# Optimization experiments

Hardware: AMD Instinct MI355X
Metric: run time of the kernel (lower is better)

## Reference

```python
import jax, jax.numpy as jnp
import numpy as np

B, S, D, F, H, E = 2, 1024, 1024, 4096, 16, 8
EPS = 1e-5


def _layernorm(x, w, b):
    m = jnp.mean(x, -1, keepdims=True)
    v = jnp.var(x, -1, keepdims=True)
    return (x - m) * jax.lax.rsqrt(v + EPS) * w + b


def _rope(x):
    # rotary embedding applied over full embed dim (split-half convention)
    b, s, d = x.shape
    half = d // 2
    inv = 1.0 / (10000.0 ** (jnp.arange(half, dtype=jnp.float32) / half))
    ang = jnp.arange(s, dtype=jnp.float32)[:, None] * inv[None, :]  # [S, half]
    cos, sin = jnp.cos(ang), jnp.sin(ang)
    x1, x2 = x[..., :half], x[..., half:]
    return jnp.concatenate([x1 * cos - x2 * sin, x1 * sin + x2 * cos], -1)


def setup_inputs() -> dict:
    key = jax.random.key(0)
    ks = jax.random.split(key, 9)
    sc = 0.02
    return {
        "x": jax.random.normal(ks[0], (B, S, D), jnp.float32),
        "ln1_w": jnp.ones((D,), jnp.float32),
        "ln1_b": jnp.zeros((D,), jnp.float32),
        "ln2_w": jnp.ones((D,), jnp.float32),
        "ln2_b": jnp.zeros((D,), jnp.float32),
        "w_qkv": jax.random.normal(ks[1], (3 * D, D), jnp.float32) * sc,
        "b_qkv": jnp.zeros((3 * D,), jnp.float32),
        "w_out": jax.random.normal(ks[2], (D, D), jnp.float32) * sc,
        "b_out": jnp.zeros((D,), jnp.float32),
        "w_router": jax.random.normal(ks[3], (D, E), jnp.float32) * sc,
        "wi": jax.random.normal(ks[4], (E, D, F), jnp.float32) * sc,  # per-expert wi (no bias)
        "wo": jax.random.normal(ks[5], (E, F // 2, D), jnp.float32) * sc,  # swiglu halves ffn dim
    }


def reference(x, ln1_w, ln1_b, ln2_w, ln2_b, w_qkv, b_qkv, w_out, b_out, w_router, wi, wo):
    # ---- pre-norm self-attention block ----
    residual = x
    h = _layernorm(x, ln1_w, ln1_b)
    h = _rope(h)
    qkv = h @ w_qkv.T + b_qkv  # [B,S,3D]
    q, k, v = jnp.split(qkv, 3, axis=-1)
    hd = D // H
    to_heads = lambda t: t.reshape(B, S, H, hd).transpose(0, 2, 1, 3)
    q, k, v = to_heads(q), to_heads(k), to_heads(v)
    scale = 1.0 / np.sqrt(hd).astype(np.float32)
    att = jax.nn.softmax(jnp.einsum('bhqd,bhkd->bhqk', q, k) * scale, axis=-1)
    o = jnp.einsum('bhqk,bhkd->bhqd', att, v).transpose(0, 2, 1, 3).reshape(B, S, D)
    o = o @ w_out.T + b_out
    x = residual + o  # attn dropout is identity at eval

    # ---- pre-norm sparse MoE FFN block ----
    residual = x
    h = _layernorm(x, ln2_w, ln2_b)
    # top-1 router in float32
    logits = h.astype(jnp.float32) @ w_router  # [B,S,E]
    probs = jax.nn.softmax(logits, axis=-1)
    mask = jax.nn.one_hot(jnp.argmax(probs, -1), E, dtype=h.dtype)  # expert_mask
    gate = probs.astype(h.dtype) * mask  # router_probs * expert_mask, [B,S,E]
    # dense all-expert compute, masked combine (same math as gather/scatter loop)
    hid = jnp.einsum('bsd,edf->bsef', h, wi)  # [B,S,E,F]
    a, g = jnp.split(hid, 2, axis=-1)
    act = jax.nn.silu(a) * g  # SwiGLU, [B,S,E,F/2]
    y = jnp.einsum('bsef,efd,bse->bsd', act, wo, gate)
    x = residual + y
    return x, logits
```

## Files before the change

kernel.cpp:

```cpp
#include <hip/hip_runtime.h>
#include <hip/hip_bf16.h>
#include <math.h>

#define BB 2
#define SS 1024
#define DD 1024
#define FF 4096
#define HH 16
#define EE 8
#define MM (BB*SS)
#define MAX_TILES 24
#define MAX_TILES2 40

typedef __attribute__((ext_vector_type(8))) short bf16x8;
typedef __attribute__((ext_vector_type(8))) short s16x8;
typedef __attribute__((ext_vector_type(4))) float f32x4;

#define OFF_WQH  ((size_t)100663296)
#define OFF_WQL  ((size_t)106954752)
#define OFF_WOH  ((size_t)113246208)
#define OFF_WOL  ((size_t)115343360)
#define OFF_H1H  ((size_t)117440512)
#define OFF_H1L  ((size_t)121634816)
#define OFF_QKV  ((size_t)125829120)
#define OFF_OH   ((size_t)150994944)
#define OFF_OL   ((size_t)155189248)
#define OFF_X2   ((size_t)159383552)
#define OFF_H2B  ((size_t)167772160)
#define OFF_ACT  ((size_t)171966464)
#define OFF_GATE ((size_t)180879360)
#define OFF_EID  ((size_t)180887552)
#define OFF_PERM ((size_t)180895744)
#define OFF_CNT  ((size_t)180903936)
#define OFF_FILL ((size_t)180903968)
#define OFF_NT   ((size_t)180904000)
#define OFF_TE   ((size_t)180904192)
#define OFF_TS   ((size_t)180904320)
#define OFF_TR   ((size_t)180904448)
#define OFF_TE2  ((size_t)180904576)
#define OFF_TS2  ((size_t)180904768)
#define OFF_TR2  ((size_t)180904960)
#define OFF_NT2  ((size_t)180905152)
#define OFF_KSH  OFF_WQH
#define OFF_KSL  (OFF_WQH + 4194304)
#define OFF_VTH  OFF_H1H
#define OFF_VTL  OFF_H1L

__device__ __forceinline__ void gload16(const void* g, void* l) {
    __builtin_amdgcn_global_load_lds(
        (const __attribute__((address_space(1))) unsigned int*)g,
        (__attribute__((address_space(3))) unsigned int*)l, 16, 0, 0);
}

__device__ __forceinline__ short bfh(float v) {
    __hip_bfloat16 h = __float2bfloat16(v);
    return *(short*)&h;
}
__device__ __forceinline__ float bf2f(short s) {
    __hip_bfloat16 h = *(__hip_bfloat16*)&s;
    return __bfloat162float(h);
}

__device__ __forceinline__ void split_write(float v, __hip_bfloat16* hp, __hip_bfloat16* lp, size_t idx) {
    __hip_bfloat16 h = __float2bfloat16(v);
    hp[idx] = h;
    lp[idx] = __float2bfloat16(v - __bfloat162float(h));
}

__global__ void k_phase0(const float* __restrict__ x, const float* __restrict__ ln1w,
                         const float* __restrict__ ln1b,
                         __hip_bfloat16* __restrict__ h1H, __hip_bfloat16* __restrict__ h1L,
                         const float* __restrict__ w_qkv, __hip_bfloat16* __restrict__ wqH,
                         __hip_bfloat16* __restrict__ wqL,
                         const float* __restrict__ w_out, __hip_bfloat16* __restrict__ woH,
                         __hip_bfloat16* __restrict__ woL) {
    __shared__ __align__(16) float smem[1032];
    int bid = blockIdx.x, t = threadIdx.x;
    if (bid < 2048) {
        int m = bid, s = m & (SS - 1);
        float* row = smem;
        float* red = smem + 1024;
        const float* xp = x + (size_t)m * DD;
        float sum = 0.f, sumsq = 0.f;
#pragma unroll
        for (int l = 0; l < 4; ++l) {
            int i = t + l * 256;
            float v = xp[i];
            row[i] = v;
            sum += v; sumsq += v * v;
        }
#pragma unroll
        for (int off = 32; off; off >>= 1) {
            sum   += __shfl_xor(sum, off);
            sumsq += __shfl_xor(sumsq, off);
        }
        int wid = t >> 6, lane = t & 63;
        if (lane == 0) { red[wid] = sum; red[4 + wid] = sumsq; }
        __syncthreads();
        sum   = red[0] + red[1] + red[2] + red[3];
        sumsq = red[4] + red[5] + red[6] + red[7];
        float mean = sum * (1.f / DD);
        float var  = sumsq * (1.f / DD) - mean * mean;
        float rstd = rsqrtf(var + 1e-5f);
        size_t base = (size_t)m * DD;
        const float kln = logf(10000.f) / 512.f;
#pragma unroll
        for (int l = 0; l < 2; ++l) {
            int i = t + l * 256;
            float n1 = (row[i]       - mean) * rstd * ln1w[i]       + ln1b[i];
            float n2 = (row[i + 512] - mean) * rstd * ln1w[i + 512] + ln1b[i + 512];
            float inv = expf(-(float)i * kln);
            float ang = (float)s * inv;
            float c = cosf(ang), sn = sinf(ang);
            split_write(n1 * c - n2 * sn,  h1H, h1L, base + i);
            split_write(n1 * sn + n2 * c, h1H, h1L, base + i + 512);
        }
    } else if (bid < 5120) {
        int idx = (bid - 2048) * 256 + t;
        float4 v = ((const float4*)w_qkv)[idx];
        split_write(v.x, wqH, wqL, (size_t)idx * 4 + 0);
        split_write(v.y, wqH, wqL, (size_t)idx * 4 + 1);
        split_write(v.z, wqH, wqL, (size_t)idx * 4 + 2);
        split_write(v.w, wqH, wqL, (size_t)idx * 4 + 3);
    } else {
        int idx = (bid - 5120) * 256 + t;
        float4 v = ((const float4*)w_out)[idx];
        split_write(v.x, woH, woL, (size_t)idx * 4 + 0);
        split_write(v.y, woH, woL, (size_t)idx * 4 + 1);
        split_write(v.z, woH, woL, (size_t)idx * 4 + 2);
        split_write(v.w, woH, woL, (size_t)idx * 4 + 3);
    }
}

__global__ void k_qkv(const __hip_bfloat16* __restrict__ Ah, const __hip_bfloat16* __restrict__ Al,
                      const __hip_bfloat16* __restrict__ Bh, const __hip_bfloat16* __restrict__ Bl,
                      const float* __restrict__ bias, float* __restrict__ Cf) {
    __shared__ __align__(16) short AsH[64 * 32];
    __shared__ __align__(16) short AsL[64 * 32];
    __shared__ __align__(16) short BsH[128 * 32];
    __shared__ __align__(16) short BsL[128 * 32];
    const int N = 3072, K = DD;
    int bid = blockIdx.x;
    int xcd = bid & 7, idx = bid >> 3;
    int nt = xcd + (idx >> 5) * 8;
    int mt = idx & 31;
    int m0 = mt * 64, n0 = nt * 128;
    const int t = threadIdx.x;
    const int w = t >> 6, lane = t & 63;
    const int sid = w * 64 + lane;
    const int g = lane >> 4, r16 = lane & 15;

    f32x4 acc[4][2] = {};

    for (int k0 = 0; k0 < K; k0 += 32) {
        {
            int rrow = sid >> 2, sl = sid & 3;
            int slog = sl ^ ((rrow >> 1) & 3);
            size_t lbase = (size_t)(w * 64) * 8;
            size_t gaoff = (size_t)(m0 + rrow) * K + k0 + slog * 8;
            gload16(Ah + gaoff, &AsH[lbase]);
            gload16(Al + gaoff, &AsL[lbase]);
        }
#pragma unroll
        for (int j = 0; j < 2; ++j) {
            int id = j * 256 + sid;
            int rrow = id >> 2, sl = id & 3;
            int slog = sl ^ ((rrow >> 1) & 3);
            size_t lbase = (size_t)(j * 256 + w * 64) * 8;
            size_t gboff = (size_t)(n0 + rrow) * K + k0 + slog * 8;
            gload16(Bh + gboff, &BsH[lbase]);
            gload16(Bl + gboff, &BsL[lbase]);
        }
        __syncthreads();
        bf16x8 ah[4], al[4], bh[2], bl[2];
#pragma unroll
        for (int i = 0; i < 4; ++i) {
            int ra = i * 16 + r16;
            int pa = g ^ ((ra >> 1) & 3);
            ah[i] = *(const bf16x8*)&AsH[ra * 32 + pa * 8];
            al[i] = *(const bf16x8*)&AsL[ra * 32 + pa * 8];
        }
#pragma unroll
        for (int n = 0; n < 2; ++n) {
            int rb = w * 32 + n * 16 + r16;
            int pb = g ^ ((rb >> 1) & 3);
            bh[n] = *(const bf16x8*)&BsH[rb * 32 + pb * 8];
            bl[n] = *(const bf16x8*)&BsL[rb * 32 + pb * 8];
        }
#pragma unroll
        for (int i = 0; i < 4; ++i)
#pragma unroll
            for (int n = 0; n < 2; ++n) {
                acc[i][n] = __builtin_amdgcn_mfma_f32_16x16x32_bf16(ah[i], bh[n], acc[i][n], 0, 0, 0);
                acc[i][n] = __builtin_amdgcn_mfma_f32_16x16x32_bf16(ah[i], bl[n], acc[i][n], 0, 0, 0);
                acc[i][n] = __builtin_amdgcn_mfma_f32_16x16x32_bf16(al[i], bh[n], acc[i][n], 0, 0, 0);
            }
        __syncthreads();
    }

#pragma unroll
    for (int i = 0; i < 4; ++i) {
#pragma unroll
        for (int n = 0; n < 2; ++n) {
            int col = n0 + w * 32 + n * 16 + r16;
#pragma unroll
            for (int q = 0; q < 4; ++q) {
                int r = m0 + i * 16 + g * 4 + q;
                Cf[(size_t)r * N + col] = acc[i][n][q] + bias[col];
            }
        }
    }
}

__global__ void k_oproj64(const __hip_bfloat16* __restrict__ Ah, const __hip_bfloat16* __restrict__ Al,
                          const __hip_bfloat16* __restrict__ Bh, const __hip_bfloat16* __restrict__ Bl,
                          const float* __restrict__ bias, const float* __restrict__ addsrc,
                          float* __restrict__ Cf, int* __restrict__ zero17) {
    __shared__ __align__(16) short AsH[64 * 32];
    __shared__ __align__(16) short AsL[64 * 32];
    __shared__ __align__(16) short BsH[128 * 32];
    __shared__ __align__(16) short BsL[128 * 32];
    const int N = DD, K = DD;
    int bid = blockIdx.x;
    int m0 = (bid >> 3) * 64, n0 = (bid & 7) * 128;
    const int t = threadIdx.x;
    if (bid == 0 && t < 17) zero17[t] = 0;
    const int w = t >> 6, lane = t & 63;
    const int sid = w * 64 + lane;
    const int g = lane >> 4, r16 = lane & 15;

    f32x4 acc[4][2] = {};

    for (int k0 = 0; k0 < K; k0 += 32) {
        {
            int rrow = sid >> 2, sl = sid & 3;
            int slog = sl ^ ((rrow >> 1) & 3);
            size_t lbase = (size_t)(w * 64) * 8;
            size_t gaoff = (size_t)(m0 + rrow) * K + k0 + slog * 8;
            gload16(Ah + gaoff, &AsH[lbase]);
            gload16(Al + gaoff, &AsL[lbase]);
        }
#pragma unroll
        for (int j = 0; j < 2; ++j) {
            int id = j * 256 + sid;
            int rrow = id >> 2, sl = id & 3;
            int slog = sl ^ ((rrow >> 1) & 3);
            size_t lbase = (size_t)(j * 256 + w * 64) * 8;
            size_t gboff = (size_t)(n0 + rrow) * K + k0 + slog * 8;
            gload16(Bh + gboff, &BsH[lbase]);
            gload16(Bl + gboff, &BsL[lbase]);
        }
        __syncthreads();
        bf16x8 ah[4], al[4], bh[2], bl[2];
#pragma unroll
        for (int i = 0; i < 4; ++i) {
            int ra = i * 16 + r16;
            int pa = g ^ ((ra >> 1) & 3);
            ah[i] = *(const bf16x8*)&AsH[ra * 32 + pa * 8];
            al[i] = *(const bf16x8*)&AsL[ra * 32 + pa * 8];
        }
#pragma unroll
        for (int n = 0; n < 2; ++n) {
            int rb = w * 32 + n * 16 + r16;
            int pb = g ^ ((rb >> 1) & 3);
            bh[n] = *(const bf16x8*)&BsH[rb * 32 + pb * 8];
            bl[n] = *(const bf16x8*)&BsL[rb * 32 + pb * 8];
        }
#pragma unroll
        for (int i = 0; i < 4; ++i)
#pragma unroll
            for (int n = 0; n < 2; ++n) {
                acc[i][n] = __builtin_amdgcn_mfma_f32_16x16x32_bf16(ah[i], bh[n], acc[i][n], 0, 0, 0);
                acc[i][n] = __builtin_amdgcn_mfma_f32_16x16x32_bf16(ah[i], bl[n], acc[i][n], 0, 0, 0);
                acc[i][n] = __builtin_amdgcn_mfma_f32_16x16x32_bf16(al[i], bh[n], acc[i][n], 0, 0, 0);
            }
        __syncthreads();
    }

#pragma unroll
    for (int i = 0; i < 4; ++i) {
#pragma unroll
        for (int n = 0; n < 2; ++n) {
            int col = n0 + w * 32 + n * 16 + r16;
#pragma unroll
            for (int q = 0; q < 4; ++q) {
                int r = m0 + i * 16 + g * 4 + q;
                Cf[(size_t)r * N + col] =
                    acc[i][n][q] + bias[col] + addsrc[(size_t)r * N + col];
            }
        }
    }
}

#define LDB 36
__global__ void k_moe_up(const __hip_bfloat16* __restrict__ A,
                         const float* __restrict__ wi,
                         __hip_bfloat16* __restrict__ act,
                         const int* __restrict__ perm,
                         const int* __restrict__ te, const int* __restrict__ ts,
                         const int* __restrict__ tr, const int* __restrict__ ntl) {
    __shared__ __align__(16) short As[128 * 32];
    __shared__ __align__(16) short Bs[128 * LDB];
    __shared__ int permS[128];
    int tile = blockIdx.y;
    if (tile >= *ntl) return;
    int e = te[tile], rs = ts[tile], rows = tr[tile];
    const int t = threadIdx.x;
    if (t < 128) permS[t] = (t < rows) ? perm[rs + t] : 0;
    __syncthreads();
    int c0 = blockIdx.x * 64;
    const int w = t >> 6, lane = t & 63;
    const int wr = w >> 1, wc = w & 1;
    const int sid = w * 64 + lane;
    const int g = lane >> 4, r16 = lane & 15;

    const float* Bp = wi + (size_t)e * DD * FF;

    const int cc = t & 127, kp0 = t >> 7;
    const int Lc = cc & 63, T = cc >> 6;
    const int qidx = (Lc >> 5) * 4 + ((Lc >> 4) & 1) * 2 + T;
    const int rbb = qidx * 16 + (Lc & 15);
    const size_t coloff = (size_t)(c0 + T * 2048 + Lc);

    f32x4 acc[4][4] = {};

    float vcur[16];
#pragma unroll
    for (int pass = 0; pass < 8; ++pass) {
        int kp = pass * 2 + kp0;
        const float* wp = Bp + (size_t)(kp * 2) * FF + coloff;
        vcur[pass * 2]     = wp[0];
        vcur[pass * 2 + 1] = wp[FF];
    }

    for (int k0 = 0; k0 < DD; k0 += 32) {
#pragma unroll
        for (int j = 0; j < 2; ++j) {
            int id = j * 256 + sid;
            int rrow = id >> 2, sl = id & 3;
            int slog = sl ^ ((rrow >> 1) & 3);
            size_t lbase = (size_t)(j * 256 + w * 64) * 8;
            gload16(A + (size_t)permS[rrow] * DD + k0 + slog * 8, &As[lbase]);
        }
#pragma unroll
        for (int pass = 0; pass < 8; ++pass) {
            int kp = pass * 2 + kp0;
            unsigned u = (unsigned)(unsigned short)bfh(vcur[pass * 2])
                       | ((unsigned)(unsigned short)bfh(vcur[pass * 2 + 1]) << 16);
            *(unsigned*)&Bs[rbb * LDB + kp * 2] = u;
        }
        __syncthreads();
        float vnext[16];
        if (k0 + 32 < DD) {
#pragma unroll
            for (int pass = 0; pass < 8; ++pass) {
                int kp = pass * 2 + kp0;
                const float* wp = Bp + (size_t)(k0 + 32 + kp * 2) * FF + coloff;
                vnext[pass * 2]     = wp[0];
                vnext[pass * 2 + 1] = wp[FF];
            }
        }
        bf16x8 af[4];
#pragma unroll
        for (int i = 0; i < 4; ++i) {
            int ra = wr * 64 + i * 16 + r16;
            int pa = g ^ ((ra >> 1) & 3);
            af[i] = *(const bf16x8*)&As[ra * 32 + pa * 8];
        }
        bf16x8 bfr[4];
#pragma unroll
        for (int n = 0; n < 4; ++n) {
            int rb = wc * 64 + n * 16 + r16;
            bfr[n] = *(const bf16x8*)&Bs[rb * LDB + g * 8];
        }
#pragma unroll
        for (int i = 0; i < 4; ++i)
#pragma unroll
            for (int n = 0; n < 4; ++n)
                acc[i][n] = __builtin_amdgcn_mfma_f32_16x16x32_bf16(af[i], bfr[n], acc[i][n], 0, 0, 0);
        __syncthreads();
        if (k0 + 32 < DD) {
#pragma unroll
            for (int j = 0; j < 16; ++j) vcur[j] = vnext[j];
        }
    }

#pragma unroll
    for (int i = 0; i < 4; ++i) {
#pragma unroll
        for (int p2 = 0; p2 < 2; ++p2) {
            int col = c0 + wc * 32 + p2 * 16 + r16;
#pragma unroll
            for (int q = 0; q < 4; ++q) {
                int r = wr * 64 + i * 16 + g * 4 + q;
                if (r < rows) {
                    float a  = acc[i][2 * p2][q];
                    float gv = acc[i][2 * p2 + 1][q];
                    act[(size_t)(rs + r) * 2048 + col] =
                        __float2bfloat16((a / (1.f + expf(-a))) * gv);
                }
            }
        }
    }
}

__global__ void k_moe_dn(const __hip_bfloat16* __restrict__ A,
                         const float* __restrict__ wo,
                         const float* __restrict__ addsrc, float* __restrict__ Cf,
                         const int* __restrict__ perm,
                         const int* __restrict__ te2, const int* __restrict__ ts2,
                         const int* __restrict__ tr2, const int* __restrict__ ntl2,
                         const float* __restrict__ gate) {
    __shared__ __align__(16) short As[64 * 32];
    __shared__ __align__(16) short Bs[64 * LDB];
    __shared__ int permS[64];
    int tile = blockIdx.y;
    if (tile >= *ntl2) return;
    int e = te2[tile], rs = ts2[tile], rows = tr2[tile];
    const int t = threadIdx.x;
    if (t < 64) permS[t] = (t < rows) ? perm[rs + t] : 0;
    __syncthreads();
    int n0 = blockIdx.x * 64;
    const int w = t >> 6, lane = t & 63;
    const int sid = w * 64 + lane;
    const int g = lane >> 4, r16 = lane & 15;
    const int K = FF / 2;

    const float* Bp = wo + (size_t)e * (size_t)K * DD;
    const int cc = t & 63, kp0 = t >> 6;

    f32x4 acc[4] = {};

    float vcur[8];
#pragma unroll
    for (int pass = 0; pass < 4; ++pass) {
        int kp = pass * 4 + kp0;
        const float* wp = Bp + (size_t)(kp * 2) * DD + n0 + cc;
        vcur[pass * 2]     = wp[0];
        vcur[pass * 2 + 1] = wp[DD];
    }

    for (int k0 = 0; k0 < K; k0 += 32) {
        {
            int rrow = sid >> 2, sl = sid & 3;
            int slog = sl ^ ((rrow >> 1) & 3);
            size_t lbase = (size_t)(w * 64) * 8;
            gload16(A + (size_t)(rs + rrow) * K + k0 + slog * 8, &As[lbase]);
        }
#pragma unroll
        for (int pass = 0; pass < 4; ++pass) {
            int kp = pass * 4 + kp0;
            unsigned u = (unsigned)(unsigned short)bfh(vcur[pass * 2])
                       | ((unsigned)(unsigned short)bfh(vcur[pass * 2 + 1]) << 16);
            *(unsigned*)&Bs[cc * LDB + kp * 2] = u;
        }
        __syncthreads();
        float vnext[8];
        if (k0 + 32 < K) {
#pragma unroll
            for (int pass = 0; pass < 4; ++pass) {
                int kp = pass * 4 + kp0;
                const float* wp = Bp + (size_t)(k0 + 32 + kp * 2) * DD + n0 + cc;
                vnext[pass * 2]     = wp[0];
                vnext[pass * 2 + 1] = wp[DD];
            }
        }
        bf16x8 af[4], bfr;
#pragma unroll
        for (int i = 0; i < 4; ++i) {
            int ra = i * 16 + r16;
            int pa = g ^ ((ra >> 1) & 3);
            af[i] = *(const bf16x8*)&As[ra * 32 + pa * 8];
        }
        {
            int rb = w * 16 + r16;
            bfr = *(const bf16x8*)&Bs[rb * LDB + g * 8];
        }
#pragma unroll
        for (int i = 0; i < 4; ++i)
            acc[i] = __builtin_amdgcn_mfma_f32_16x16x32_bf16(af[i], bfr, acc[i], 0, 0, 0);
        __syncthreads();
        if (k0 + 32 < K) {
#pragma unroll
            for (int j = 0; j < 8; ++j) vcur[j] = vnext[j];
        }
    }

#pragma unroll
    for (int i = 0; i < 4; ++i) {
        int col = n0 + w * 16 + r16;
#pragma unroll
        for (int q = 0; q < 4; ++q) {
            int r = i * 16 + g * 4 + q;
            if (r >= rows) continue;
            int tok = permS[r];
            Cf[(size_t)tok * DD + col] = addsrc[(size_t)tok * DD + col] + gate[tok] * acc[i][q];
        }
    }
}

__global__ void k_prep(const float* __restrict__ qkv, short* __restrict__ KH, short* __restrict__ KL,
                       short* __restrict__ VH, short* __restrict__ VL) {
    __shared__ float tile[64][65];
    int b = blockIdx.z, h = blockIdx.y, s0 = blockIdx.x * 64;
    int t = threadIdx.x;
    int row = t >> 2, c0 = (t & 3) * 16;
    const float* kp = qkv + (size_t)(b * SS + s0 + row) * 3072 + 1024 + h * 64 + c0;
    const float* vp = kp + 1024;
    {
        size_t krow = ((size_t)(b * HH + h) * SS + s0 + row) * 64;
        int key = (s0 + row) & 7;
#pragma unroll
        for (int g2 = 0; g2 < 2; ++g2) {
            s16x8 hv, lv;
#pragma unroll
            for (int j = 0; j < 8; ++j) {
                float v = kp[g2 * 8 + j];
                short hh = bfh(v);
                hv[j] = hh; lv[j] = bfh(v - bf2f(hh));
            }
            int p = ((c0 >> 3) + g2) ^ key;
            *(s16x8*)&KH[krow + p * 8] = hv;
            *(s16x8*)&KL[krow + p * 8] = lv;
        }
    }
#pragma unroll
    for (int j = 0; j < 16; ++j) tile[row][c0 + j] = vp[j];
    __syncthreads();
    {
        int d = t >> 2, sc = (t & 3) * 16;
        size_t vrow = ((size_t)(b * HH + h) * 64 + d) * SS + s0;
        int key = d & 7;
#pragma unroll
        for (int g2 = 0; g2 < 2; ++g2) {
            s16x8 hv, lv;
#pragma unroll
            for (int j = 0; j < 8; ++j) {
                float v = tile[sc + g2 * 8 + j][d];
                short hh = bfh(v);
                hv[j] = hh; lv[j] = bfh(v - bf2f(hh));
            }
            int p = ((sc >> 3) + g2) ^ key;
            *(s16x8*)&VH[vrow + p * 8] = hv;
            *(s16x8*)&VL[vrow + p * 8] = lv;
        }
    }
}

#define LDP 72
__global__ __launch_bounds__(512, 1)
void k_attn_mfma(const float* __restrict__ qkv,
                 const short* __restrict__ KH, const short* __restrict__ KL,
                 const short* __restrict__ VH, const short* __restrict__ VL,
                 __hip_bfloat16* __restrict__ ohi, __hip_bfloat16* __restrict__ olo) {
    __shared__ __align__(16) short Ks[2][64 * 64], Kl2[2][64 * 64], Vs[2][64 * 64], Vl2[2][64 * 64];
    __shared__ __align__(16) short PhS[8][16 * LDP], PlS[8][16 * LDP];
    int id = blockIdx.x;
    int xcd = id & 7, slot = id >> 3;
    int bh = xcd * 4 + (slot >> 3);
    int q0 = (slot & 7) * 128;
    int b = bh >> 4, h = bh & 15;
    int t = threadIdx.x;
    int w = t >> 6, lane = t & 63;
    int g = lane >> 4, r16 = lane & 15;
    int srow = t >> 3, sslot = t & 7;

    const size_t kbase = ((size_t)bh * SS) * 64;
    const size_t vbase = ((size_t)bh * 64) * SS;

    bf16x8 qfh[2], qfl[2];
    {
        const float* qp = qkv + (size_t)(b * SS + q0 + w * 16 + r16) * 3072 + h * 64;
#pragma unroll
        for (int ks = 0; ks < 2; ++ks) {
            float vv[8];
            *(float4*)&vv[0] = *(const float4*)(qp + ks * 32 + g * 8);
            *(float4*)&vv[4] = *(const float4*)(qp + ks * 32 + g * 8 + 4);
#pragma unroll
            for (int j = 0; j < 8; ++j) {
                float sv = vv[j] * 0.125f;
                short hh = bfh(sv);
                qfh[ks][j] = hh;
                qfl[ks][j] = bfh(sv - bf2f(hh));
            }
        }
    }

    float mrun[4], lrun[4];
    f32x4 oacc[4] = {};
#pragma unroll
    for (int q = 0; q < 4; ++q) { mrun[q] = -1e30f; lrun[q] = 0.f; }

    gload16(KH + kbase + (size_t)srow * 64 + sslot * 8, &Ks[0][w * 512]);
    gload16(KL + kbase + (size_t)srow * 64 + sslot * 8, &Kl2[0][w * 512]);
    gload16(VH + vbase + (size_t)srow * SS + sslot * 8, &Vs[0][w * 512]);
    gload16(VL + vbase + (size_t)srow * SS + sslot * 8, &Vl2[0][w * 512]);
    __syncthreads();

    int cur = 0;
    for (int k0 = 0; k0 < SS; k0 += 64) {
        if (k0 + 64 < SS) {
            int kn = k0 + 64;
            gload16(KH + kbase + (size_t)(kn + srow) * 64 + sslot * 8, &Ks[cur ^ 1][w * 512]);
            gload16(KL + kbase + (size_t)(kn + srow) * 64 + sslot * 8, &Kl2[cur ^ 1][w * 512]);
            gload16(VH + vbase + (size_t)srow * SS + kn + sslot * 8,   &Vs[cur ^ 1][w * 512]);
            gload16(VL + vbase + (size_t)srow * SS + kn + sslot * 8,   &Vl2[cur ^ 1][w * 512]);
        }

        f32x4 accs[4] = {};
#pragma unroll
        for (int ks = 0; ks < 2; ++ks) {
            bf16x8 kfh[4], kfl[4];
#pragma unroll
            for (int n = 0; n < 4; ++n) {
                int rb = n * 16 + r16;
                int p = (ks * 4 + g) ^ (r16 & 7);
                kfh[n] = *(const bf16x8*)&Ks[cur][rb * 64 + p * 8];
                kfl[n] = *(const bf16x8*)&Kl2[cur][rb * 64 + p * 8];
            }
            __builtin_amdgcn_s_setprio(1);
#pragma unroll
            for (int n = 0; n < 4; ++n) {
                accs[n] = __builtin_amdgcn_mfma_f32_16x16x32_bf16(qfh[ks], kfh[n], accs[n], 0, 0, 0);
                accs[n] = __builtin_amdgcn_mfma_f32_16x16x32_bf16(qfh[ks], kfl[n], accs[n], 0, 0, 0);
                accs[n] = __builtin_amdgcn_mfma_f32_16x16x32_bf16(qfl[ks], kfh[n], accs[n], 0, 0, 0);
            }
            __builtin_amdgcn_s_setprio(0);
        }

        float mn[4], corr[4], psum[4];
#pragma unroll
        for (int q = 0; q < 4; ++q) {
            float m = fmaxf(fmaxf(accs[0][q], accs[1][q]), fmaxf(accs[2][q], accs[3][q]));
            m = fmaxf(m, __shfl_xor(m, 1));
            m = fmaxf(m, __shfl_xor(m, 2));
            m = fmaxf(m, __shfl_xor(m, 4));
            m = fmaxf(m, __shfl_xor(m, 8));
            mn[q] = fmaxf(mrun[q], m);
            corr[q] = expf(mrun[q] - mn[q]);
            mrun[q] = mn[q];
            psum[q] = 0.f;
        }
#pragma unroll
        for (int n = 0; n < 4; ++n)
#pragma unroll
            for (int q = 0; q < 4; ++q) {
                float p = expf(accs[n][q] - mn[q]);
                psum[q] += p;
                short ph = bfh(p);
                PhS[w][(g * 4 + q) * LDP + n * 16 + r16] = ph;
                PlS[w][(g * 4 + q) * LDP + n * 16 + r16] = bfh(p - bf2f(ph));
            }
#pragma unroll
        for (int q = 0; q < 4; ++q) {
            psum[q] += __shfl_xor(psum[q], 1);
            psum[q] += __shfl_xor(psum[q], 2);
            psum[q] += __shfl_xor(psum[q], 4);
            psum[q] += __shfl_xor(psum[q], 8);
            lrun[q] = lrun[q] * corr[q] + psum[q];
#pragma unroll
            for (int n = 0; n < 4; ++n) oacc[n][q] *= corr[q];
        }

#pragma unroll
        for (int ks = 0; ks < 2; ++ks) {
            bf16x8 vfh[4], vfl[4];
#pragma unroll
            for (int n = 0; n < 4; ++n) {
                int rb = n * 16 + r16;
                int p = (ks * 4 + g) ^ (r16 & 7);
                vfh[n] = *(const bf16x8*)&Vs[cur][rb * 64 + p * 8];
                vfl[n] = *(const bf16x8*)&Vl2[cur][rb * 64 + p * 8];
            }
            bf16x8 pfh = *(const bf16x8*)&PhS[w][r16 * LDP + ks * 32 + g * 8];
            bf16x8 pfl = *(const bf16x8*)&PlS[w][r16 * LDP + ks * 32 + g * 8];
            __builtin_amdgcn_s_setprio(1);
#pragma unroll
            for (int n = 0; n < 4; ++n) {
                oacc[n] = __builtin_amdgcn_mfma_f32_16x16x32_bf16(pfh, vfh[n], oacc[n], 0, 0, 0);
                oacc[n] = __builtin_amdgcn_mfma_f32_16x16x32_bf16(pfh, vfl[n], oacc[n], 0, 0, 0);
                oacc[n] = __builtin_amdgcn_mfma_f32_16x16x32_bf16(pfl, vfh[n], oacc[n], 0, 0, 0);
            }
            __builtin_amdgcn_s_setprio(0);
        }
        __syncthreads();
        cur ^= 1;
    }

    float invl[4];
#pragma unroll
    for (int q = 0; q < 4; ++q) invl[q] = 1.f / lrun[q];
#pragma unroll
    for (int n = 0; n < 4; ++n) {
        int col = h * 64 + n * 16 + r16;
#pragma unroll
        for (int q = 0; q < 4; ++q) {
            int rowg = b * SS + q0 + w * 16 + g * 4 + q;
            split_write(oacc[n][q] * invl[q], ohi, olo, (size_t)rowg * DD + col);
        }
    }
}

__global__ void k_ln2_router(const float* __restrict__ x2, const float* __restrict__ w,
                             const float* __restrict__ b, const float* __restrict__ wr,
                             __hip_bfloat16* __restrict__ h2b, float* __restrict__ logits,
                             float* __restrict__ gate, int* __restrict__ eid,
                             int* __restrict__ counts) {
    int m = blockIdx.x, t = threadIdx.x;
    __shared__ float red[8];
    __shared__ float racc[4][8];
    const float* xp = x2 + (size_t)m * DD;
    float v[4];
    float sum = 0.f, sumsq = 0.f;
#pragma unroll
    for (int l = 0; l < 4; ++l) {
        v[l] = xp[t + l * 256];
        sum += v[l]; sumsq += v[l] * v[l];
    }
#pragma unroll
    for (int off = 32; off; off >>= 1) {
        sum   += __shfl_xor(sum, off);
        sumsq += __shfl_xor(sumsq, off);
    }
    int wid = t >> 6, lane = t & 63;
    if (lane == 0) { red[wid] = sum; red[4 + wid] = sumsq; }
    __syncthreads();
    sum   = red[0] + red[1] + red[2] + red[3];
    sumsq = red[4] + red[5] + red[6] + red[7];
    float mean = sum * (1.f / DD);
    float var  = sumsq * (1.f / DD) - mean * mean;
    float rstd = rsqrtf(var + 1e-5f);
    float acc[EE] = {};
#pragma unroll
    for (int l = 0; l < 4; ++l) {
        int i = t + l * 256;
        float hv = (v[l] - mean) * rstd * w[i] + b[i];
        h2b[(size_t)m * DD + i] = __float2bfloat16(hv);
        const float* wp = wr + (size_t)i * EE;
#pragma unroll
        for (int n = 0; n < EE; ++n) acc[n] += hv * wp[n];
    }
#pragma unroll
    for (int off = 32; off; off >>= 1)
#pragma unroll
        for (int n = 0; n < EE; ++n) acc[n] += __shfl_xor(acc[n], off);
    if (lane == 0)
#pragma unroll
        for (int n = 0; n < EE; ++n) racc[wid][n] = acc[n];
    __syncthreads();
    if (t == 0) {
        float lg[EE];
#pragma unroll
        for (int n = 0; n < EE; ++n) lg[n] = racc[0][n] + racc[1][n] + racc[2][n] + racc[3][n];
        float mx = lg[0]; int best = 0;
#pragma unroll
        for (int n = 1; n < EE; ++n) if (lg[n] > mx) { mx = lg[n]; best = n; }
        float den = 0.f;
#pragma unroll
        for (int n = 0; n < EE; ++n) den += expf(lg[n] - mx);
        gate[m] = 1.f / den;
        eid[m] = best;
        atomicAdd(&counts[best], 1);
#pragma unroll
        for (int n = 0; n < EE; ++n) logits[(size_t)m * EE + n] = lg[n];
    }
}

__global__ void k_offscatter(const int* __restrict__ counts,
                             int* __restrict__ te, int* __restrict__ ts, int* __restrict__ tr,
                             int* __restrict__ ntl,
                             int* __restrict__ te2, int* __restrict__ ts2, int* __restrict__ tr2,
                             int* __restrict__ ntl2,
                             const int* __restrict__ eid,
                             int* __restrict__ fill, int* __restrict__ perm) {
    __shared__ int soffs[EE];
    int t = threadIdx.x;
    if (t == 0) {
        int off = 0, nt = 0, nt2 = 0;
        for (int e = 0; e < EE; ++e) {
            soffs[e] = off;
            int c = counts[e];
            for (int t0 = 0; t0 < c; t0 += 128) {
                te[nt] = e; ts[nt] = off + t0; tr[nt] = (c - t0 < 128) ? (c - t0) : 128; ++nt;
            }
            for (int t0 = 0; t0 < c; t0 += 64) {
                te2[nt2] = e; ts2[nt2] = off + t0; tr2[nt2] = (c - t0 < 64) ? (c - t0) : 64; ++nt2;
            }
            off += c;
        }
        *ntl = nt;
        *ntl2 = nt2;
    }
    __syncthreads();
#pragma unroll
    for (int tok = t; tok < MM; tok += 1024) {
        int e = eid[tok];
        int pos = soffs[e] + atomicAdd(&fill[e], 1);
        perm[pos] = tok;
    }
}

extern "C" void kernel_launch(void* const* d_in, const int* in_sizes, int n_in,
                              void* d_out, int out_size, void* d_ws, size_t ws_size,
                              hipStream_t stream) {
    const float* x     = (const float*)d_in[0];
    const float* ln1w  = (const float*)d_in[1];
    const float* ln1b  = (const float*)d_in[2];
    const float* ln2w  = (const float*)d_in[3];
    const float* ln2b  = (const float*)d_in[4];
    const float* w_qkv = (const float*)d_in[5];
    const float* b_qkv = (const float*)d_in[6];
    const float* w_out = (const float*)d_in[7];
    const float* b_out = (const float*)d_in[8];
    const float* w_rtr = (const float*)d_in[9];
    const float* wi    = (const float*)d_in[10];
    const float* wo    = (const float*)d_in[11];
    float* out = (float*)d_out;

    char* wsb = (char*)d_ws;
    __hip_bfloat16* wqH  = (__hip_bfloat16*)(wsb + OFF_WQH);
    __hip_bfloat16* wqL  = (__hip_bfloat16*)(wsb + OFF_WQL);
    __hip_bfloat16* woH  = (__hip_bfloat16*)(wsb + OFF_WOH);
    __hip_bfloat16* woL  = (__hip_bfloat16*)(wsb + OFF_WOL);
    __hip_bfloat16* h1H  = (__hip_bfloat16*)(wsb + OFF_H1H);
    __hip_bfloat16* h1L  = (__hip_bfloat16*)(wsb + OFF_H1L);
    float*          qkvF = (float*)(wsb + OFF_QKV);
    __hip_bfloat16* oH   = (__hip_bfloat16*)(wsb + OFF_OH);
    __hip_bfloat16* oL   = (__hip_bfloat16*)(wsb + OFF_OL);
    float*          x2F  = (float*)(wsb + OFF_X2);
    __hip_bfloat16* h2B  = (__hip_bfloat16*)(wsb + OFF_H2B);
    __hip_bfloat16* actB = (__hip_bfloat16*)(wsb + OFF_ACT);
    short* KSH = (short*)(wsb + OFF_KSH);
    short* KSL = (short*)(wsb + OFF_KSL);
    short* VTH = (short*)(wsb + OFF_VTH);
    short* VTL = (short*)(wsb + OFF_VTL);
    float* gate = (float*)(wsb + OFF_GATE);
    int* eid    = (int*)(wsb + OFF_EID);
    int* perm   = (int*)(wsb + OFF_PERM);
    int* counts = (int*)(wsb + OFF_CNT);
    int* fill   = (int*)(wsb + OFF_FILL);
    int* ntl    = (int*)(wsb + OFF_NT);
    int* te     = (int*)(wsb + OFF_TE);
    int* tsx    = (int*)(wsb + OFF_TS);
    int* trx    = (int*)(wsb + OFF_TR);
    int* te2    = (int*)(wsb + OFF_TE2);
    int* ts2    = (int*)(wsb + OFF_TS2);
    int* tr2    = (int*)(wsb + OFF_TR2);
    int* ntl2   = (int*)(wsb + OFF_NT2);

    k_phase0<<<6144, 256, 0, stream>>>(x, ln1w, ln1b, h1H, h1L, w_qkv, wqH, wqL,
                                       w_out, woH, woL);
    k_qkv<<<768, 256, 0, stream>>>(h1H, h1L, wqH, wqL, b_qkv, qkvF);
    k_prep<<<dim3(SS / 64, HH, BB), 256, 0, stream>>>(qkvF, KSH, KSL, VTH, VTL);
    k_attn_mfma<<<256, 512, 0, stream>>>(qkvF, KSH, KSL, VTH, VTL, oH, oL);
    k_oproj64<<<256, 256, 0, stream>>>(oH, oL, woH, woL, b_out, x, x2F, counts);
    k_ln2_router<<<MM, 256, 0, stream>>>(x2F, ln2w, ln2b, w_rtr, h2B,
                                         out + (size_t)MM * DD, gate, eid, counts);
    k_offscatter<<<1, 1024, 0, stream>>>(counts, te, tsx, trx, ntl,
                                         te2, ts2, tr2, ntl2, eid, fill, perm);
    k_moe_up<<<dim3(32, MAX_TILES), 256, 0, stream>>>(h2B, wi, actB, perm, te, tsx, trx, ntl);
    k_moe_dn<<<dim3(DD / 64, MAX_TILES2), 256, 0, stream>>>(
        actB, wo, x2F, out, perm, te2, ts2, tr2, ntl2, gate);
}
```

Measured before the change: 331.7 us.

## Use 64-row expert tiles in MoE up-projection and double K-step per barrier

The MoE up-projection switches from 128-row token tiles to the 64-row tile list used by the down-projection. This gives more blocks and less padding waste when experts receive few tokens, but each wi weight tile is now reloaded for more tiles. Both MoE GEMMs now stage 64 K-elements per loop iteration across two LDS panels, halving the number of barriers. The cost is more registers for the prefetched weight values and more shared memory.

Result: faster. 320.9 us (-3.3%).

```diff
diff --git a/kernel.cpp b/kernel.cpp
--- a/kernel.cpp
+++ b/kernel.cpp
@@ -297,21 +297,19 @@
                          const float* __restrict__ wi,
                          __hip_bfloat16* __restrict__ act,
                          const int* __restrict__ perm,
-                         const int* __restrict__ te, const int* __restrict__ ts,
-                         const int* __restrict__ tr, const int* __restrict__ ntl) {
-    __shared__ __align__(16) short As[128 * 32];
-    __shared__ __align__(16) short Bs[128 * LDB];
-    __shared__ int permS[128];
+                         const int* __restrict__ te2, const int* __restrict__ ts2,
+                         const int* __restrict__ tr2, const int* __restrict__ ntl2) {
+    __shared__ __align__(16) short As[2][64 * 32];
+    __shared__ __align__(16) short Bs[2][128 * LDB];
+    __shared__ int permS[64];
     int tile = blockIdx.y;
-    if (tile >= *ntl) return;
-    int e = te[tile], rs = ts[tile], rows = tr[tile];
+    if (tile >= *ntl2) return;
+    int e = te2[tile], rs = ts2[tile], rows = tr2[tile];
     const int t = threadIdx.x;
-    if (t < 128) permS[t] = (t < rows) ? perm[rs + t] : 0;
+    if (t < 64) permS[t] = (t < rows) ? perm[rs + t] : 0;
     __syncthreads();
     int c0 = blockIdx.x * 64;
     const int w = t >> 6, lane = t & 63;
-    const int wr = w >> 1, wc = w & 1;
-    const int sid = w * 64 + lane;
     const int g = lane >> 4, r16 = lane & 15;
 
     const float* Bp = wi + (size_t)e * DD * FF;
@@ -322,80 +320,81 @@
     const int rbb = qidx * 16 + (Lc & 15);
     const size_t coloff = (size_t)(c0 + T * 2048 + Lc);
 
-    f32x4 acc[4][4] = {};
-
-    float vcur[16];
-#pragma unroll
-    for (int pass = 0; pass < 8; ++pass) {
-        int kp = pass * 2 + kp0;
-        const float* wp = Bp + (size_t)(kp * 2) * FF + coloff;
+    f32x4 acc[4][2] = {};
+
+    float vcur[32];
+#pragma unroll
+    for (int pass = 0; pass < 16; ++pass) {
+        int kpg = pass * 2 + kp0;
+        const float* wp = Bp + (size_t)(kpg * 2) * FF + coloff;
         vcur[pass * 2]     = wp[0];
         vcur[pass * 2 + 1] = wp[FF];
     }
 
-    for (int k0 = 0; k0 < DD; k0 += 32) {
+    for (int k0 = 0; k0 < DD; k0 += 64) {
 #pragma unroll
         for (int j = 0; j < 2; ++j) {
-            int id = j * 256 + sid;
-            int rrow = id >> 2, sl = id & 3;
+            int rrow = t >> 2, sl = t & 3;
             int slog = sl ^ ((rrow >> 1) & 3);
-            size_t lbase = (size_t)(j * 256 + w * 64) * 8;
-            gload16(A + (size_t)permS[rrow] * DD + k0 + slog * 8, &As[lbase]);
-        }
-#pragma unroll
-        for (int pass = 0; pass < 8; ++pass) {
-            int kp = pass * 2 + kp0;
+            size_t lbase = (size_t)(w * 64) * 8;
+            gload16(A + (size_t)permS[rrow] * DD + k0 + j * 32 + slog * 8, &As[j][lbase]);
+        }
+#pragma unroll
+        for (int pass = 0; pass < 16; ++pass) {
+            int kpg = pass * 2 + kp0;
+            int panel = kpg >> 4, kpl = kpg & 15;
             unsigned u = (unsigned)(unsigned short)bfh(vcur[pass * 2])
                        | ((unsigned)(unsigned short)bfh(vcur[pass * 2 + 1]) << 16);
-            *(unsigned*)&Bs[rbb * LDB + kp * 2] = u;
-        }
-        __syncthreads();
-        float vnext[16];
-        if (k0 + 32 < DD) {
-#pragma unroll
-            for (int pass = 0; pass < 8; ++pass) {
-                int kp = pass * 2 + kp0;
-                const float* wp = Bp + (size_t)(k0 + 32 + kp * 2) * FF + coloff;
+            *(unsigned*)&Bs[panel][rbb * LDB + kpl * 2] = u;
+        }
+        __syncthreads();
+        float vnext[32];
+        if (k0 + 64 < DD) {
+#pragma unroll
+            for (int pass = 0; pass < 16; ++pass) {
+                int kpg = pass * 2 + kp0;
+                const float* wp = Bp + (size_t)(k0 + 64 + kpg * 2) * FF + coloff;
                 vnext[pass * 2]     = wp[0];
                 vnext[pass * 2 + 1] = wp[FF];
             }
         }
-        bf16x8 af[4];
+#pragma unroll
+        for (int ks = 0; ks < 2; ++ks) {
+            bf16x8 af[4], bf[2];
+#pragma unroll
+            for (int i = 0; i < 4; ++i) {
+                int ra = i * 16 + r16;
+                int pa = g ^ ((ra >> 1) & 3);
+                af[i] = *(const bf16x8*)&As[ks][ra * 32 + pa * 8];
+            }
+#pragma unroll
+            for (int n = 0; n < 2; ++n) {
+                int rb = w * 32 + n * 16 + r16;
+                bf[n] = *(const bf16x8*)&Bs[ks][rb * LDB + g * 8];
+            }
+#pragma unroll
+            for (int i = 0; i < 4; ++i)
+#pragma unroll
+                for (int n = 0; n < 2; ++n)
+                    acc[i][n] = __builtin_amdgcn_mfma_f32_16x16x32_bf16(af[i], bf[n], acc[i][n], 0, 0, 0);
+        }
+        __syncthreads();
+        if (k0 + 64 < DD) {
+#pragma unroll
+            for (int j = 0; j < 32; ++j) vcur[j] = vnext[j];
+        }
+    }
+
+    {
+        int col = c0 + (w >> 1) * 32 + (w & 1) * 16 + r16;
 #pragma unroll
         for (int i = 0; i < 4; ++i) {
-            int ra = wr * 64 + i * 16 + r16;
-            int pa = g ^ ((ra >> 1) & 3);
-            af[i] = *(const bf16x8*)&As[ra * 32 + pa * 8];
-        }
-        bf16x8 bfr[4];
-#pragma unroll
-        for (int n = 0; n < 4; ++n) {
-            int rb = wc * 64 + n * 16 + r16;
-            bfr[n] = *(const bf16x8*)&Bs[rb * LDB + g * 8];
-        }
-#pragma unroll
-        for (int i = 0; i < 4; ++i)
-#pragma unroll
-            for (int n = 0; n < 4; ++n)
-                acc[i][n] = __builtin_amdgcn_mfma_f32_16x16x32_bf16(af[i], bfr[n], acc[i][n], 0, 0, 0);
-        __syncthreads();
-        if (k0 + 32 < DD) {
-#pragma unroll
-            for (int j = 0; j < 16; ++j) vcur[j] = vnext[j];
-        }
-    }
-
-#pragma unroll
-    for (int i = 0; i < 4; ++i) {
-#pragma unroll
-        for (int p2 = 0; p2 < 2; ++p2) {
-            int col = c0 + wc * 32 + p2 * 16 + r16;
 #pragma unroll
             for (int q = 0; q < 4; ++q) {
-                int r = wr * 64 + i * 16 + g * 4 + q;
+                int r = i * 16 + g * 4 + q;
                 if (r < rows) {
-                    float a  = acc[i][2 * p2][q];
-                    float gv = acc[i][2 * p2 + 1][q];
+                    float a  = acc[i][0][q];
+                    float gv = acc[i][1][q];
                     act[(size_t)(rs + r) * 2048 + col] =
                         __float2bfloat16((a / (1.f + expf(-a))) * gv);
                 }
@@ -411,8 +410,8 @@
                          const int* __restrict__ te2, const int* __restrict__ ts2,
                          const int* __restrict__ tr2, const int* __restrict__ ntl2,
                          const float* __restrict__ gate) {
-    __shared__ __align__(16) short As[64 * 32];
-    __shared__ __align__(16) short Bs[64 * LDB];
+    __shared__ __align__(16) short As[2][64 * 32];
+    __shared__ __align__(16) short Bs[2][64 * LDB];
     __shared__ int permS[64];
     int tile = blockIdx.y;
     if (tile >= *ntl2) return;
@@ -422,7 +421,6 @@
     __syncthreads();
     int n0 = blockIdx.x * 64;
     const int w = t >> 6, lane = t & 63;
-    const int sid = w * 64 + lane;
     const int g = lane >> 4, r16 = lane & 15;
     const int K = FF / 2;
 
@@ -431,58 +429,63 @@
 
     f32x4 acc[4] = {};
 
-    float vcur[8];
-#pragma unroll
-    for (int pass = 0; pass < 4; ++pass) {
-        int kp = pass * 4 + kp0;
-        const float* wp = Bp + (size_t)(kp * 2) * DD + n0 + cc;
+    float vcur[16];
+#pragma unroll
+    for (int pass = 0; pass < 8; ++pass) {
+        int kpg = pass * 4 + kp0;
+        const float* wp = Bp + (size_t)(kpg * 2) * DD + n0 + cc;
         vcur[pass * 2]     = wp[0];
         vcur[pass * 2 + 1] = wp[DD];
     }
 
-    for (int k0 = 0; k0 < K; k0 += 32) {
-        {
-            int rrow = sid >> 2, sl = sid & 3;
+    for (int k0 = 0; k0 < K; k0 += 64) {
+#pragma unroll
+        for (int j = 0; j < 2; ++j) {
+            int rrow = t >> 2, sl = t & 3;
             int slog = sl ^ ((rrow >> 1) & 3);
             size_t lbase = (size_t)(w * 64) * 8;
-            gload16(A + (size_t)(rs + rrow) * K + k0 + slog * 8, &As[lbase]);
-        }
-#pragma unroll
-        for (int pass = 0; pass < 4; ++pass) {
-            int kp = pass * 4 + kp0;
+            gload16(A + (size_t)(rs + rrow) * K + k0 + j * 32 + slog * 8, &As[j][lbase]);
+        }
+#pragma unroll
+        for (int pass = 0; pass < 8; ++pass) {
+            int kpg = pass * 4 + kp0;
+            int panel = kpg >> 4, kpl = kpg & 15;
             unsigned u = (unsigned)(unsigned short)bfh(vcur[pass * 2])
                        | ((unsigned)(unsigned short)bfh(vcur[pass * 2 + 1]) << 16);
-            *(unsigned*)&Bs[cc * LDB + kp * 2] = u;
-        }
-        __syncthreads();
-        float vnext[8];
-        if (k0 + 32 < K) {
-#pragma unroll
-            for (int pass = 0; pass < 4; ++pass) {
-                int kp = pass * 4 + kp0;
-                const float* wp = Bp + (size_t)(k0 + 32 + kp * 2) * DD + n0 + cc;
+            *(unsigned*)&Bs[panel][cc * LDB + kpl * 2] = u;
+        }
+        __syncthreads();
+        float vnext[16];
+        if (k0 + 64 < K) {
+#pragma unroll
+            for (int pass = 0; pass < 8; ++pass) {
+                int kpg = pass * 4 + kp0;
+                const float* wp = Bp + (size_t)(k0 + 64 + kpg * 2) * DD + n0 + cc;
                 vnext[pass * 2]     = wp[0];
                 vnext[pass * 2 + 1] = wp[DD];
             }
         }
-        bf16x8 af[4], bfr;
-#pragma unroll
-        for (int i = 0; i < 4; ++i) {
-            int ra = i * 16 + r16;
-            int pa = g ^ ((ra >> 1) & 3);
-            af[i] = *(const bf16x8*)&As[ra * 32 + pa * 8];
-        }
-        {
-            int rb = w * 16 + r16;
-            bfr = *(const bf16x8*)&Bs[rb * LDB + g * 8];
-        }
-#pragma unroll
-        for (int i = 0; i < 4; ++i)
-            acc[i] = __builtin_amdgcn_mfma_f32_16x16x32_bf16(af[i], bfr, acc[i], 0, 0, 0);
-        __syncthreads();
-        if (k0 + 32 < K) {
-#pragma unroll
-            for (int j = 0; j < 8; ++j) vcur[j] = vnext[j];
+#pragma unroll
+        for (int ks = 0; ks < 2; ++ks) {
+            bf16x8 af[4], bfr;
+#pragma unroll
+            for (int i = 0; i < 4; ++i) {
+                int ra = i * 16 + r16;
+                int pa = g ^ ((ra >> 1) & 3);
+                af[i] = *(const bf16x8*)&As[ks][ra * 32 + pa * 8];
+            }
+            {
+                int rb = w * 16 + r16;
+                bfr = *(const bf16x8*)&Bs[ks][rb * LDB + g * 8];
+            }
+#pragma unroll
+            for (int i = 0; i < 4; ++i)
+                acc[i] = __builtin_amdgcn_mfma_f32_16x16x32_bf16(af[i], bfr, acc[i], 0, 0, 0);
+        }
+        __syncthreads();
+        if (k0 + 64 < K) {
+#pragma unroll
+            for (int j = 0; j < 16; ++j) vcur[j] = vnext[j];
         }
     }
 
@@ -858,7 +861,7 @@
                                          out + (size_t)MM * DD, gate, eid, counts);
     k_offscatter<<<1, 1024, 0, stream>>>(counts, te, tsx, trx, ntl,
                                          te2, ts2, tr2, ntl2, eid, fill, perm);
-    k_moe_up<<<dim3(32, MAX_TILES), 256, 0, stream>>>(h2B, wi, actB, perm, te, tsx, trx, ntl);
+    k_moe_up<<<dim3(32, MAX_TILES2), 256, 0, stream>>>(h2B, wi, actB, perm, te2, ts2, tr2, ntl2);
     k_moe_dn<<<dim3(DD / 64, MAX_TILES2), 256, 0, stream>>>(
         actB, wo, x2F, out, perm, te2, ts2, tr2, ntl2, gate);
 }
```
